# Kernel optimization log

Measured on AMD Instinct MI355X. Metric: run time of the kernel, lower is better.

The kernel has to match this reference:

```python
import jax, jax.numpy as jnp
import numpy as np

B, S, E, H = 2, 2048, 1024, 16
D = E // H  # head dim = 64


def setup_inputs() -> dict:
    key = jax.random.key(0)
    ks = jax.random.split(key, 6)
    x = jax.random.normal(ks[0], (B, S, E), dtype=jnp.float32)
    attn_mask = jax.random.bernoulli(ks[1], 0.1, (B, S, S))  # True = masked
    scale = 1.0 / np.sqrt(E)
    w_kernel = jax.random.normal(ks[2], (E, 3 * E), dtype=jnp.float32) * scale
    w_bias = jax.random.normal(ks[3], (3 * E,), dtype=jnp.float32) * 0.02
    fc_kernel = jax.random.normal(ks[4], (E, E), dtype=jnp.float32) * scale
    fc_bias = jax.random.normal(ks[5], (E,), dtype=jnp.float32) * 0.02
    return {"x": x, "attn_mask": attn_mask, "w_kernel": w_kernel,
            "w_bias": w_bias, "fc_kernel": fc_kernel, "fc_bias": fc_bias}


def reference(x, attn_mask, w_kernel, w_bias, fc_kernel, fc_bias):
    b, s, e = x.shape
    qkv = jnp.einsum("bse,ef->bsf", x, w_kernel) + w_bias  # (B,S,3E)
    q, k, v = jnp.split(qkv, 3, axis=-1)

    def heads(t):  # (B,S,E) -> (B,H,S,D)
        return t.reshape(b, s, H, D).transpose(0, 2, 1, 3)

    q, k, v = heads(q), heads(k), heads(v)
    scores = jnp.einsum("bhqd,bhkd->bhqk", q, k) / jnp.sqrt(jnp.float32(D))
    # faithful quirk: masked positions are filled with 1e-9, not -inf
    scores = jnp.where(attn_mask[:, None, :, :], jnp.float32(1e-9), scores)
    A = jax.nn.softmax(scores, axis=-1)
    out = jnp.einsum("bhqk,bhkd->bhqd", A, v)  # (B,H,S,D)
    out = out.transpose(0, 2, 1, 3).reshape(b, s, e)
    # dropout is identity in eval mode
    return jnp.einsum("bse,ef->bsf", out, fc_kernel) + fc_bias
```

## Files before the change

kernel.cpp:

```cpp
#include <hip/hip_runtime.h>
#include <math.h>

#define BB 2
#define SS 2048
#define EE 1024
#define HH 16

typedef _Float16 f16;
typedef __attribute__((ext_vector_type(8))) _Float16 f16x8;
typedef __attribute__((ext_vector_type(4))) _Float16 f16x4;
typedef __attribute__((ext_vector_type(2))) _Float16 f16x2;
typedef __attribute__((ext_vector_type(4))) float f32x4;

union P8 { f16x8 v8; f16x2 h2[4]; };
union V8 { f16x8 v8; f16x4 v4[2]; };

#define QSCALE 0.18033688011112042f

#if __has_builtin(__builtin_amdgcn_exp2f)
#define EXP2(x) __builtin_amdgcn_exp2f(x)
#else
#define EXP2(x) exp2f(x)
#endif

static __device__ __forceinline__ f16x2 pk2(float a, float b) {
#if __has_builtin(__builtin_amdgcn_cvt_pkrtz)
  return __builtin_bit_cast(f16x2, __builtin_amdgcn_cvt_pkrtz(a, b));
#else
  f16x2 r; r[0] = (f16)a; r[1] = (f16)b; return r;
#endif
}

static __device__ __forceinline__ void gl16(const void* g, void* l) {
  __builtin_amdgcn_global_load_lds(
      (const __attribute__((address_space(1))) void*)g,
      (__attribute__((address_space(3))) void*)l, 16, 0, 0);
}

__global__ __launch_bounds__(256) void cvt_f32_f16(
    const float* __restrict__ in, f16* __restrict__ out, int n)
{
  int i = (blockIdx.x * 256 + threadIdx.x) * 8;
  if (i >= n) return;
  float4 a = *(const float4*)(in + i);
  float4 b = *(const float4*)(in + i + 4);
  f16x8 o;
  o[0] = (f16)a.x; o[1] = (f16)a.y; o[2] = (f16)a.z; o[3] = (f16)a.w;
  o[4] = (f16)b.x; o[5] = (f16)b.y; o[6] = (f16)b.z; o[7] = (f16)b.w;
  *(f16x8*)(out + i) = o;
}

__global__ __launch_bounds__(256) void transpose_cvt(
    const float* __restrict__ in, f16* __restrict__ out, int K, int N)
{
  __shared__ float T[64][65];
  const int k0 = blockIdx.y * 64, n0 = blockIdx.x * 64;
  const int tr = threadIdx.x >> 4, tc = (threadIdx.x & 15) * 4;
#pragma unroll
  for (int i = 0; i < 4; ++i) {
    int r = tr + i * 16;
    *(float4*)&T[r][tc] = *(const float4*)(in + (size_t)(k0 + r) * N + n0 + tc);
  }
  __syncthreads();
#pragma unroll
  for (int i = 0; i < 4; ++i) {
    int nl = tr + i * 16;
    f16x4 v;
    v[0] = (f16)T[tc + 0][nl];
    v[1] = (f16)T[tc + 1][nl];
    v[2] = (f16)T[tc + 2][nl];
    v[3] = (f16)T[tc + 3][nl];
    *(f16x4*)(out + (size_t)(n0 + nl) * K + k0 + tc) = v;
  }
}

__global__ __launch_bounds__(256) void pack_mask(
    const int* __restrict__ m, unsigned long long* __restrict__ bits)
{
  const int i = blockIdx.x * 256 + threadIdx.x;
  const unsigned long long bal = __ballot(m[i] != 0);
  if ((threadIdx.x & 63) == 0) bits[i >> 6] = bal;
}

__global__ __launch_bounds__(256) void gemm_f16(
    const f16* __restrict__ A, const f16* __restrict__ Bt,
    const float* __restrict__ bias, int M, int N, int K, int mode,
    f16* __restrict__ oQK, f16* __restrict__ oVT, float* __restrict__ oF32)
{
  __shared__ f16 Ah[128 * 32];
  __shared__ f16 Bh[128 * 32];

  const int t = threadIdx.x;
  const int l = t & 63, w = t >> 6;
  const int l15 = l & 15, l4 = l >> 4;
  const int wr = w >> 1, wc = w & 1;
  const int n0 = blockIdx.x * 128, m0 = blockIdx.y * 128;

  const int srow = l >> 2;
  const int gch  = (l & 3) ^ (srow & 3);
  const f16* Ap0 = A + (size_t)(m0 + w * 32 + srow) * K + gch * 8;
  const f16* Ap1 = Ap0 + (size_t)16 * K;
  const f16* Bp0 = Bt + (size_t)(n0 + w * 32 + srow) * K + gch * 8;
  const f16* Bp1 = Bp0 + (size_t)16 * K;
  f16* ldsA0 = &Ah[(w * 32) * 32];
  f16* ldsA1 = &Ah[(w * 32 + 16) * 32];
  f16* ldsB0 = &Bh[(w * 32) * 32];
  f16* ldsB1 = &Bh[(w * 32 + 16) * 32];

  f32x4 acc[4][4] = {};
  const int csw = (l15 & 3);

  for (int k0 = 0; k0 < K; k0 += 32) {
    gl16(Ap0 + k0, ldsA0);
    gl16(Ap1 + k0, ldsA1);
    gl16(Bp0 + k0, ldsB0);
    gl16(Bp1 + k0, ldsB1);
    __syncthreads();

    f16x8 af[4], bf[4];
#pragma unroll
    for (int mr = 0; mr < 4; ++mr) {
      const int row = wr * 64 + mr * 16 + l15;
      af[mr] = *(const f16x8*)&Ah[row * 32 + ((l4 ^ csw) * 8)];
    }
#pragma unroll
    for (int nr = 0; nr < 4; ++nr) {
      const int row = wc * 64 + nr * 16 + l15;
      bf[nr] = *(const f16x8*)&Bh[row * 32 + ((l4 ^ csw) * 8)];
    }
    __builtin_amdgcn_s_setprio(1);
#pragma unroll
    for (int mr = 0; mr < 4; ++mr)
#pragma unroll
      for (int nr = 0; nr < 4; ++nr)
        acc[mr][nr] = __builtin_amdgcn_mfma_f32_16x16x32_f16(
            af[mr], bf[nr], acc[mr][nr], 0, 0, 0);
    __builtin_amdgcn_s_setprio(0);
    __syncthreads();
  }

  if (mode == 1) {
#pragma unroll
    for (int nr = 0; nr < 4; ++nr) {
      const int n = n0 + wc * 64 + nr * 16 + l15;
      const float bv = bias[n];
#pragma unroll
      for (int mr = 0; mr < 4; ++mr)
#pragma unroll
        for (int j = 0; j < 4; ++j) {
          const int m = m0 + wr * 64 + mr * 16 + l4 * 4 + j;
          oF32[(size_t)m * N + n] = acc[mr][nr][j] + bv;
        }
    }
  } else {
#pragma unroll
    for (int nr = 0; nr < 4; ++nr) {
      const int n = n0 + wc * 64 + nr * 16 + l15;
      const float bv = bias[n];
      if (n < 2048) {
        const float qs = (n < 1024) ? QSCALE : 1.0f;
#pragma unroll
        for (int mr = 0; mr < 4; ++mr)
#pragma unroll
          for (int j = 0; j < 4; ++j) {
            const int m = m0 + wr * 64 + mr * 16 + l4 * 4 + j;
            oQK[(size_t)m * 2048 + n] = (f16)((acc[mr][nr][j] + bv) * qs);
          }
      } else {
        const int hh = (n - 2048) >> 6;
        const int d = (n - 2048) & 63;
#pragma unroll
        for (int mr = 0; mr < 4; ++mr) {
          const int tok0 = m0 + wr * 64 + mr * 16 + l4 * 4;
          const int bq = tok0 >> 11, sq = tok0 & 2047;
          f16x4 v;
          v[0] = (f16)(acc[mr][nr][0] + bv);
          v[1] = (f16)(acc[mr][nr][1] + bv);
          v[2] = (f16)(acc[mr][nr][2] + bv);
          v[3] = (f16)(acc[mr][nr][3] + bv);
          *(f16x4*)(oVT + ((size_t)(bq * 16 + hh) * 64 + d) * SS + sq) = v;
        }
      }
    }
  }
}

__global__ __launch_bounds__(256, 2) void attn_mfma(
    const f16* __restrict__ qkbuf, const f16* __restrict__ vT,
    const unsigned long long* __restrict__ mbits,
    f16* __restrict__ Opart, float* __restrict__ Lpart)
{
  __shared__ f16 Kds[2][64 * 64];
  __shared__ f16 Vds[2][64 * 64];

  const int t = threadIdx.x;
  const int w = t >> 6, l = t & 63, l15 = l & 15, l4 = l >> 4;
  const int bh = blockIdx.y, b = bh >> 4, h = bh & 15;
  const int ks = blockIdx.z;
  const int qbase = blockIdx.x * 128 + w * 32;

  f16x8 q00, q01, q10, q11;
  {
    const size_t r0 = (size_t)(b * SS + qbase + l15) * 2048 + h * 64;
    const size_t r1 = (size_t)(b * SS + qbase + 16 + l15) * 2048 + h * 64;
    q00 = *(const f16x8*)(qkbuf + r0 + l4 * 8);
    q01 = *(const f16x8*)(qkbuf + r0 + 32 + l4 * 8);
    q10 = *(const f16x8*)(qkbuf + r1 + l4 * 8);
    q11 = *(const f16x8*)(qkbuf + r1 + 32 + l4 * 8);
  }

  f32x4 accA[4] = {}, accB[4] = {};
  f32x4 accLA = {}, accLB = {};
  f16x8 ones;
#pragma unroll
  for (int i = 0; i < 8; ++i) ones[i] = (f16)1.0f;

  const unsigned long long* mA =
      mbits + (size_t)(b * SS + qbase + l15) * 32 + ks * 16;
  const unsigned long long* mB =
      mbits + (size_t)(b * SS + qbase + 16 + l15) * 32 + ks * 16;

  const int srow = t >> 3;
  const int scb  = (t & 7) * 8;
  const int sws  = (srow & 7) << 3;
  const f16* kb = qkbuf + (size_t)b * SS * 2048 + 1024 + h * 64 + scb +
                  (size_t)ks * 1024 * 2048;
  const f16* vb = vT + ((size_t)bh * 64 + srow) * SS + scb + ks * 1024;

  f16x8 kr0, kr1, vr0, vr1;
#define LOADT(kt)                                                         \
  {                                                                       \
    kr0 = *(const f16x8*)(kb + (size_t)((kt) + srow) * 2048);             \
    kr1 = *(const f16x8*)(kb + (size_t)((kt) + srow + 32) * 2048);        \
    vr0 = *(const f16x8*)(vb + (kt));                                     \
    vr1 = *(const f16x8*)(vb + 32 * SS + (kt));                           \
  }
#define COMMIT(bi)                                                        \
  {                                                                       \
    *(f16x8*)&Kds[bi][srow * 64 + (scb ^ sws)]        = kr0;              \
    *(f16x8*)&Kds[bi][(srow + 32) * 64 + (scb ^ sws)] = kr1;              \
    *(f16x8*)&Vds[bi][srow * 64 + (scb ^ sws)]        = vr0;              \
    *(f16x8*)&Vds[bi][(srow + 32) * 64 + (scb ^ sws)] = vr1;              \
  }

  LOADT(0)
  COMMIT(0)
  LOADT(64)
  __syncthreads();

  const int swr = (l15 & 7) << 3;

#define BODY(cur, tI)                                                         \
  {                                                                           \
    const unsigned long long mbA = mA[tI];                                    \
    const unsigned long long mbB = mB[tI];                                    \
    _Pragma("unroll")                                                         \
    for (int sg = 0; sg < 2; ++sg) {                                          \
      float pA[8], pB[8];                                                     \
      _Pragma("unroll")                                                       \
      for (int gh = 0; gh < 2; ++gh) {                                        \
        const int g = sg * 2 + gh;                                            \
        const f16* krow = &Kds[cur][(g * 16 + l15) * 64];                     \
        const f16x8 k0 = *(const f16x8*)(krow + ((l4 * 8) ^ swr));            \
        const f16x8 k1 = *(const f16x8*)(krow + ((32 + l4 * 8) ^ swr));       \
        __builtin_amdgcn_s_setprio(1);                                        \
        f32x4 SA = __builtin_amdgcn_mfma_f32_16x16x32_f16(                    \
            k0, q00, (f32x4){0.f, 0.f, 0.f, 0.f}, 0, 0, 0);                   \
        SA = __builtin_amdgcn_mfma_f32_16x16x32_f16(k1, q01, SA, 0, 0, 0);    \
        f32x4 SB = __builtin_amdgcn_mfma_f32_16x16x32_f16(                    \
            k0, q10, (f32x4){0.f, 0.f, 0.f, 0.f}, 0, 0, 0);                   \
        SB = __builtin_amdgcn_mfma_f32_16x16x32_f16(k1, q11, SB, 0, 0, 0);    \
        __builtin_amdgcn_s_setprio(0);                                        \
        const unsigned int nibA = (unsigned int)(mbA >> (g * 16 + l4 * 4));   \
        const unsigned int nibB = (unsigned int)(mbB >> (g * 16 + l4 * 4));   \
        _Pragma("unroll")                                                     \
        for (int j = 0; j < 4; ++j) {                                         \
          pA[gh * 4 + j] = ((nibA >> j) & 1u) ? 1.0f : EXP2(SA[j]);           \
          pB[gh * 4 + j] = ((nibB >> j) & 1u) ? 1.0f : EXP2(SB[j]);           \
        }                                                                     \
      }                                                                       \
      P8 uA, uB;                                                              \
      uA.h2[0] = pk2(pA[0], pA[1]); uA.h2[1] = pk2(pA[2], pA[3]);             \
      uA.h2[2] = pk2(pA[4], pA[5]); uA.h2[3] = pk2(pA[6], pA[7]);             \
      uB.h2[0] = pk2(pB[0], pB[1]); uB.h2[1] = pk2(pB[2], pB[3]);             \
      uB.h2[2] = pk2(pB[4], pB[5]); uB.h2[3] = pk2(pB[6], pB[7]);             \
      __builtin_amdgcn_s_setprio(1);                                          \
      _Pragma("unroll")                                                       \
      for (int dg = 0; dg < 4; ++dg) {                                        \
        const f16* vrow = &Vds[cur][(dg * 16 + l15) * 64];                    \
        V8 uv;                                                                \
        uv.v4[0] = *(const f16x4*)(vrow + ((sg * 32 + l4 * 4) ^ swr));        \
        uv.v4[1] = *(const f16x4*)(vrow + ((sg * 32 + 16 + l4 * 4) ^ swr));   \
        accA[dg] = __builtin_amdgcn_mfma_f32_16x16x32_f16(uA.v8, uv.v8,       \
                                                          accA[dg], 0, 0, 0); \
        accB[dg] = __builtin_amdgcn_mfma_f32_16x16x32_f16(uB.v8, uv.v8,       \
                                                          accB[dg], 0, 0, 0); \
      }                                                                       \
      accLA = __builtin_amdgcn_mfma_f32_16x16x32_f16(uA.v8, ones, accLA,      \
                                                     0, 0, 0);                \
      accLB = __builtin_amdgcn_mfma_f32_16x16x32_f16(uB.v8, ones, accLB,      \
                                                     0, 0, 0);                \
      __builtin_amdgcn_s_setprio(0);                                          \
    }                                                                         \
    if ((tI) + 1 < 16) {                                                      \
      COMMIT((cur) ^ 1)                                                       \
      if ((tI) + 2 < 16) LOADT(((tI) + 2) * 64)                               \
    }                                                                         \
    __syncthreads();                                                          \
  }

  for (int tI = 0; tI < 16; tI += 2) {
    BODY(0, tI)
    BODY(1, tI + 1)
  }

  const size_t obase = (size_t)ks * 4096 * EE;
#pragma unroll
  for (int j = 0; j < 4; ++j) {
    const int qr = l4 * 4 + j;
    const size_t rowA = (size_t)(b * SS + qbase + qr) * EE + h * 64 + l15;
    const size_t rowB = (size_t)(b * SS + qbase + 16 + qr) * EE + h * 64 + l15;
#pragma unroll
    for (int dg = 0; dg < 4; ++dg) {
      Opart[obase + rowA + dg * 16] = (f16)accA[dg][j];
      Opart[obase + rowB + dg * 16] = (f16)accB[dg][j];
    }
    if (l15 == 0) {
      Lpart[(size_t)ks * 4096 * HH + (size_t)(b * SS + qbase + qr) * HH + h] =
          accLA[j];
      Lpart[(size_t)ks * 4096 * HH +
            (size_t)(b * SS + qbase + 16 + qr) * HH + h] = accLB[j];
    }
  }
}

__global__ __launch_bounds__(256) void combine(
    const f16* __restrict__ Opart, const float* __restrict__ Lpart,
    f16* __restrict__ aout)
{
  const size_t i = ((size_t)blockIdx.x * 256 + threadIdx.x) * 8;
  const int token = (int)(i >> 10);
  const int h = (int)((i >> 6) & 15);
  const float inv =
      1.0f / (Lpart[(size_t)token * HH + h] +
              Lpart[(size_t)4096 * HH + (size_t)token * HH + h]);
  const f16x8 o0 = *(const f16x8*)(Opart + i);
  const f16x8 o1 = *(const f16x8*)(Opart + (size_t)4096 * EE + i);
  f16x8 o;
#pragma unroll
  for (int j = 0; j < 8; ++j)
    o[j] = (f16)(((float)o0[j] + (float)o1[j]) * inv);
  *(f16x8*)(aout + i) = o;
}

extern "C" void kernel_launch(void* const* d_in, const int* in_sizes, int n_in,
                              void* d_out, int out_size, void* d_ws,
                              size_t ws_size, hipStream_t stream)
{
  (void)in_sizes; (void)n_in; (void)out_size; (void)ws_size;
  const float* x   = (const float*)d_in[0];
  const int* mask  = (const int*)d_in[1];
  const float* wk  = (const float*)d_in[2];
  const float* wb  = (const float*)d_in[3];
  const float* fck = (const float*)d_in[4];
  const float* fcb = (const float*)d_in[5];
  float* out       = (float*)d_out;

  char* ws = (char*)d_ws;
  f16* fckT = (f16*)(ws);
  f16* qk   = (f16*)(ws + 2097152);
  f16* vT   = (f16*)(ws + 18874368);
  unsigned long long* mbits = (unsigned long long*)(ws + 27262976);
  float* Lp = (float*)(ws + 28311552);
  char* scratch = ws + 28835840;
  f16* xh    = (f16*)scratch;
  f16* Wt    = (f16*)(scratch + 8388608);
  f16* Opart = (f16*)scratch;
  f16* aoutH = qk;

  cvt_f32_f16<<<4096 * 1024 / (8 * 256), 256, 0, stream>>>(x, xh, 4096 * 1024);
  transpose_cvt<<<dim3(3072 / 64, 1024 / 64), 256, 0, stream>>>(wk, Wt, 1024, 3072);
  transpose_cvt<<<dim3(1024 / 64, 1024 / 64), 256, 0, stream>>>(fck, fckT, 1024, 1024);
  pack_mask<<<BB * SS * SS / 256, 256, 0, stream>>>(mask, mbits);

  gemm_f16<<<dim3(3072 / 128, 4096 / 128), 256, 0, stream>>>(
      xh, Wt, wb, 4096, 3072, 1024, 0, qk, vT, nullptr);

  attn_mfma<<<dim3(SS / 128, BB * HH, 2), 256, 0, stream>>>(
      qk, vT, mbits, Opart, Lp);
  combine<<<4096 * 1024 / (8 * 256), 256, 0, stream>>>(Opart, Lp, aoutH);

  gemm_f16<<<dim3(1024 / 128, 4096 / 128), 256, 0, stream>>>(
      aoutH, fckT, fcb, 4096, 1024, 1024, 1, nullptr, nullptr, out);
}
```

Measured before the change: 253.6 us.

## Halve attention K/V tile to 32 keys and raise occupancy to 4 blocks

Shrinks the per-iteration key tile from 64 to 32, which halves LDS use and the staging registers, and raises launch bounds from 2 to 4 blocks per CU. V is stored with a padded row stride of 36 instead of an XOR swizzle, and the mask is read as 32-bit words. The goal is more resident waves to hide memory latency. In exchange the kernel runs twice as many barrier-synchronised iterations with less work per barrier.

```diff
diff --git a/kernel.cpp b/kernel.cpp
--- a/kernel.cpp
+++ b/kernel.cpp
@@ -185,13 +185,14 @@
   }
 }
 
-__global__ __launch_bounds__(256, 2) void attn_mfma(
+#define VPAD 36
+__global__ __launch_bounds__(256, 4) void attn_mfma(
     const f16* __restrict__ qkbuf, const f16* __restrict__ vT,
     const unsigned long long* __restrict__ mbits,
     f16* __restrict__ Opart, float* __restrict__ Lpart)
 {
-  __shared__ f16 Kds[2][64 * 64];
-  __shared__ f16 Vds[2][64 * 64];
+  __shared__ f16 Kds[2][32 * 64];
+  __shared__ f16 Vds[2][64 * VPAD];
 
   const int t = threadIdx.x;
   const int w = t >> 6, l = t & 63, l15 = l & 15, l4 = l >> 4;
@@ -215,101 +216,96 @@
 #pragma unroll
   for (int i = 0; i < 8; ++i) ones[i] = (f16)1.0f;
 
-  const unsigned long long* mA =
-      mbits + (size_t)(b * SS + qbase + l15) * 32 + ks * 16;
-  const unsigned long long* mB =
-      mbits + (size_t)(b * SS + qbase + 16 + l15) * 32 + ks * 16;
+  const unsigned int* mA =
+      (const unsigned int*)mbits + (size_t)(b * SS + qbase + l15) * 64 + ks * 32;
+  const unsigned int* mB =
+      (const unsigned int*)mbits + (size_t)(b * SS + qbase + 16 + l15) * 64 + ks * 32;
 
   const int srow = t >> 3;
   const int scb  = (t & 7) * 8;
   const int sws  = (srow & 7) << 3;
   const f16* kb = qkbuf + (size_t)b * SS * 2048 + 1024 + h * 64 + scb +
                   (size_t)ks * 1024 * 2048;
-  const f16* vb = vT + ((size_t)bh * 64 + srow) * SS + scb + ks * 1024;
-
-  f16x8 kr0, kr1, vr0, vr1;
+  const int vd  = t >> 2;
+  const int vkb = (t & 3) * 8;
+  const f16* vb = vT + ((size_t)bh * 64 + vd) * SS + ks * 1024 + vkb;
+
+  f16x8 kr0; V8 vr0;
 #define LOADT(kt)                                                         \
   {                                                                       \
     kr0 = *(const f16x8*)(kb + (size_t)((kt) + srow) * 2048);             \
-    kr1 = *(const f16x8*)(kb + (size_t)((kt) + srow + 32) * 2048);        \
-    vr0 = *(const f16x8*)(vb + (kt));                                     \
-    vr1 = *(const f16x8*)(vb + 32 * SS + (kt));                           \
+    vr0.v8 = *(const f16x8*)(vb + (kt));                                  \
   }
 #define COMMIT(bi)                                                        \
   {                                                                       \
-    *(f16x8*)&Kds[bi][srow * 64 + (scb ^ sws)]        = kr0;              \
-    *(f16x8*)&Kds[bi][(srow + 32) * 64 + (scb ^ sws)] = kr1;              \
-    *(f16x8*)&Vds[bi][srow * 64 + (scb ^ sws)]        = vr0;              \
-    *(f16x8*)&Vds[bi][(srow + 32) * 64 + (scb ^ sws)] = vr1;              \
+    *(f16x8*)&Kds[bi][srow * 64 + (scb ^ sws)] = kr0;                     \
+    *(f16x4*)&Vds[bi][vd * VPAD + vkb]     = vr0.v4[0];                   \
+    *(f16x4*)&Vds[bi][vd * VPAD + vkb + 4] = vr0.v4[1];                   \
   }
 
   LOADT(0)
   COMMIT(0)
-  LOADT(64)
+  LOADT(32)
   __syncthreads();
 
   const int swr = (l15 & 7) << 3;
 
 #define BODY(cur, tI)                                                         \
   {                                                                           \
-    const unsigned long long mbA = mA[tI];                                    \
-    const unsigned long long mbB = mB[tI];                                    \
+    const unsigned int mbA = mA[tI];                                          \
+    const unsigned int mbB = mB[tI];                                          \
+    float pA[8], pB[8];                                                       \
     _Pragma("unroll")                                                         \
-    for (int sg = 0; sg < 2; ++sg) {                                          \
-      float pA[8], pB[8];                                                     \
+    for (int g = 0; g < 2; ++g) {                                             \
+      const f16* krow = &Kds[cur][(g * 16 + l15) * 64];                       \
+      const f16x8 k0 = *(const f16x8*)(krow + ((l4 * 8) ^ swr));              \
+      const f16x8 k1 = *(const f16x8*)(krow + ((32 + l4 * 8) ^ swr));         \
+      __builtin_amdgcn_s_setprio(1);                                          \
+      f32x4 SA = __builtin_amdgcn_mfma_f32_16x16x32_f16(                      \
+          k0, q00, (f32x4){0.f, 0.f, 0.f, 0.f}, 0, 0, 0);                     \
+      SA = __builtin_amdgcn_mfma_f32_16x16x32_f16(k1, q01, SA, 0, 0, 0);      \
+      f32x4 SB = __builtin_amdgcn_mfma_f32_16x16x32_f16(                      \
+          k0, q10, (f32x4){0.f, 0.f, 0.f, 0.f}, 0, 0, 0);                     \
+      SB = __builtin_amdgcn_mfma_f32_16x16x32_f16(k1, q11, SB, 0, 0, 0);      \
+      __builtin_amdgcn_s_setprio(0);                                          \
+      const unsigned int nibA = mbA >> (g * 16 + l4 * 4);                     \
+      const unsigned int nibB = mbB >> (g * 16 + l4 * 4);                     \
       _Pragma("unroll")                                                       \
-      for (int gh = 0; gh < 2; ++gh) {                                        \
-        const int g = sg * 2 + gh;                                            \
-        const f16* krow = &Kds[cur][(g * 16 + l15) * 64];                     \
-        const f16x8 k0 = *(const f16x8*)(krow + ((l4 * 8) ^ swr));            \
-        const f16x8 k1 = *(const f16x8*)(krow + ((32 + l4 * 8) ^ swr));       \
-        __builtin_amdgcn_s_setprio(1);                                        \
-        f32x4 SA = __builtin_amdgcn_mfma_f32_16x16x32_f16(                    \
-            k0, q00, (f32x4){0.f, 0.f, 0.f, 0.f}, 0, 0, 0);                   \
-        SA = __builtin_amdgcn_mfma_f32_16x16x32_f16(k1, q01, SA, 0, 0, 0);    \
-        f32x4 SB = __builtin_amdgcn_mfma_f32_16x16x32_f16(                    \
-            k0, q10, (f32x4){0.f, 0.f, 0.f, 0.f}, 0, 0, 0);                   \
-        SB = __builtin_amdgcn_mfma_f32_16x16x32_f16(k1, q11, SB, 0, 0, 0);    \
-        __builtin_amdgcn_s_setprio(0);                                        \
-        const unsigned int nibA = (unsigned int)(mbA >> (g * 16 + l4 * 4));   \
-        const unsigned int nibB = (unsigned int)(mbB >> (g * 16 + l4 * 4));   \
-        _Pragma("unroll")                                                     \
-        for (int j = 0; j < 4; ++j) {                                         \
-          pA[gh * 4 + j] = ((nibA >> j) & 1u) ? 1.0f : EXP2(SA[j]);           \
-          pB[gh * 4 + j] = ((nibB >> j) & 1u) ? 1.0f : EXP2(SB[j]);           \
-        }                                                                     \
+      for (int j = 0; j < 4; ++j) {                                           \
+        pA[g * 4 + j] = ((nibA >> j) & 1u) ? 1.0f : EXP2(SA[j]);              \
+        pB[g * 4 + j] = ((nibB >> j) & 1u) ? 1.0f : EXP2(SB[j]);              \
       }                                                                       \
-      P8 uA, uB;                                                              \
-      uA.h2[0] = pk2(pA[0], pA[1]); uA.h2[1] = pk2(pA[2], pA[3]);             \
-      uA.h2[2] = pk2(pA[4], pA[5]); uA.h2[3] = pk2(pA[6], pA[7]);             \
-      uB.h2[0] = pk2(pB[0], pB[1]); uB.h2[1] = pk2(pB[2], pB[3]);             \
-      uB.h2[2] = pk2(pB[4], pB[5]); uB.h2[3] = pk2(pB[6], pB[7]);             \
-      __builtin_amdgcn_s_setprio(1);                                          \
-      _Pragma("unroll")                                                       \
-      for (int dg = 0; dg < 4; ++dg) {                                        \
-        const f16* vrow = &Vds[cur][(dg * 16 + l15) * 64];                    \
-        V8 uv;                                                                \
-        uv.v4[0] = *(const f16x4*)(vrow + ((sg * 32 + l4 * 4) ^ swr));        \
-        uv.v4[1] = *(const f16x4*)(vrow + ((sg * 32 + 16 + l4 * 4) ^ swr));   \
-        accA[dg] = __builtin_amdgcn_mfma_f32_16x16x32_f16(uA.v8, uv.v8,       \
-                                                          accA[dg], 0, 0, 0); \
-        accB[dg] = __builtin_amdgcn_mfma_f32_16x16x32_f16(uB.v8, uv.v8,       \
-                                                          accB[dg], 0, 0, 0); \
-      }                                                                       \
-      accLA = __builtin_amdgcn_mfma_f32_16x16x32_f16(uA.v8, ones, accLA,      \
-                                                     0, 0, 0);                \
-      accLB = __builtin_amdgcn_mfma_f32_16x16x32_f16(uB.v8, ones, accLB,      \
-                                                     0, 0, 0);                \
-      __builtin_amdgcn_s_setprio(0);                                          \
     }                                                                         \
-    if ((tI) + 1 < 16) {                                                      \
+    P8 uA, uB;                                                                \
+    uA.h2[0] = pk2(pA[0], pA[1]); uA.h2[1] = pk2(pA[2], pA[3]);               \
+    uA.h2[2] = pk2(pA[4], pA[5]); uA.h2[3] = pk2(pA[6], pA[7]);               \
+    uB.h2[0] = pk2(pB[0], pB[1]); uB.h2[1] = pk2(pB[2], pB[3]);               \
+    uB.h2[2] = pk2(pB[4], pB[5]); uB.h2[3] = pk2(pB[6], pB[7]);               \
+    __builtin_amdgcn_s_setprio(1);                                            \
+    _Pragma("unroll")                                                         \
+    for (int dg = 0; dg < 4; ++dg) {                                          \
+      const f16* vrow = &Vds[cur][(dg * 16 + l15) * VPAD];                    \
+      V8 uv;                                                                  \
+      uv.v4[0] = *(const f16x4*)(vrow + l4 * 4);                              \
+      uv.v4[1] = *(const f16x4*)(vrow + 16 + l4 * 4);                         \
+      accA[dg] = __builtin_amdgcn_mfma_f32_16x16x32_f16(uA.v8, uv.v8,         \
+                                                        accA[dg], 0, 0, 0);   \
+      accB[dg] = __builtin_amdgcn_mfma_f32_16x16x32_f16(uB.v8, uv.v8,         \
+                                                        accB[dg], 0, 0, 0);   \
+    }                                                                         \
+    accLA = __builtin_amdgcn_mfma_f32_16x16x32_f16(uA.v8, ones, accLA,        \
+                                                   0, 0, 0);                  \
+    accLB = __builtin_amdgcn_mfma_f32_16x16x32_f16(uB.v8, ones, accLB,        \
+                                                   0, 0, 0);                  \
+    __builtin_amdgcn_s_setprio(0);                                            \
+    if ((tI) + 1 < 32) {                                                      \
       COMMIT((cur) ^ 1)                                                       \
-      if ((tI) + 2 < 16) LOADT(((tI) + 2) * 64)                               \
+      if ((tI) + 2 < 32) LOADT(((tI) + 2) * 32)                               \
     }                                                                         \
     __syncthreads();                                                          \
   }
 
-  for (int tI = 0; tI < 16; tI += 2) {
+  for (int tI = 0; tI < 32; tI += 2) {
     BODY(0, tI)
     BODY(1, tI + 1)
   }
```

New measurement: 243.3 us. -4.1%, faster.
